# Performance work log

Measured on AMD Instinct MI355X. Metric: run time of the kernel, lower is better.

The kernel has to match this reference:

```python
import jax, jax.numpy as jnp
import numpy as np

NUM_HEADS = 30
EPS = 1e-5


def _fp32_layernorm(x):
    # LayerNorm over last dim, no affine, computed in fp32 (FP32LayerNorm)
    xf = x.astype(jnp.float32)
    mu = jnp.mean(xf, axis=-1, keepdims=True)
    var = jnp.mean(jnp.square(xf - mu), axis=-1, keepdims=True)
    return ((xf - mu) * jax.lax.rsqrt(var + EPS)).astype(x.dtype)


def _apply_rotary(x, cos, sin):
    # x: [B,H,S,hd]; cos/sin: [S,hd] -> broadcast via [None,None]
    half = x.shape[-1] // 2
    xr, xi = x[..., :half], x[..., half:]
    x_rot = jnp.concatenate([-xi, xr], axis=-1)
    out = x.astype(jnp.float32) * cos[None, None] + x_rot.astype(jnp.float32) * sin[None, None]
    return out.astype(x.dtype)


def setup_inputs() -> dict:
    key = jax.random.key(0)
    ks = jax.random.split(key, 12)
    B, S_img, S_txt, D = 1, 3072, 256, 1920
    hd = D // NUM_HEADS
    s = 0.02
    return {
        "hidden_states": jax.random.normal(ks[0], (B, S_img, D), jnp.float32),
        "encoder_hidden_states": jax.random.normal(ks[1], (B, S_txt, D), jnp.float32),
        "rope_cos": jax.random.normal(ks[2], (S_img, hd), jnp.float32),
        "rope_sin": jax.random.normal(ks[3], (S_img, hd), jnp.float32),
        "Wq": jax.random.normal(ks[4], (D, D), jnp.float32) * s,
        "bq": jnp.zeros((D,), jnp.float32),
        "Wk": jax.random.normal(ks[5], (D, D), jnp.float32) * s,
        "bk": jnp.zeros((D,), jnp.float32),
        "Wv": jax.random.normal(ks[6], (D, D), jnp.float32) * s,
        "bv": jnp.zeros((D,), jnp.float32),
        "Wo": jax.random.normal(ks[7], (D, D), jnp.float32) * s,
        "bo": jnp.zeros((D,), jnp.float32),
    }


def reference(hidden_states, encoder_hidden_states, rope_cos, rope_sin,
              Wq, bq, Wk, bk, Wv, bv, Wo, bo):
    T = encoder_hidden_states.shape[1]  # text_seq_length
    x = jnp.concatenate([encoder_hidden_states, hidden_states], axis=1)  # [B,S,D]
    B, S, D = x.shape
    H = NUM_HEADS
    hd = D // H

    def proj(W, b):
        return (x @ W.T + b).reshape(B, S, H, hd).transpose(0, 2, 1, 3)  # [B,H,S,hd]

    q = _fp32_layernorm(proj(Wq, bq))
    k = _fp32_layernorm(proj(Wk, bk))
    v = proj(Wv, bv)

    # partial RoPE: only the image slice (tokens after text)
    q = q.at[:, :, T:, :].set(_apply_rotary(q[:, :, T:, :], rope_cos, rope_sin))
    k = k.at[:, :, T:, :].set(_apply_rotary(k[:, :, T:, :], rope_cos, rope_sin))

    scale = 1.0 / jnp.sqrt(jnp.asarray(hd, q.dtype))
    scores = jnp.einsum("bhqd,bhkd->bhqk", q, k) * scale
    attn = jax.nn.softmax(scores, axis=-1)
    out = jnp.einsum("bhqk,bhkd->bhqd", attn, v)  # [B,H,S,hd]

    out = out.transpose(0, 2, 1, 3).reshape(B, S, D)
    out = out @ Wo.T + bo
    return (out[:, T:], out[:, :T])  # (image hidden_states, encoder_hidden_states)
```

## Files before the change

kernel.cpp:

```cpp
#include <hip/hip_runtime.h>

constexpr int S_TOT  = 3328;
constexpr int S_TXT  = 256;
constexpr int DMODEL = 1920;
constexpr int NHEAD  = 30;
constexpr int HD     = 64;

typedef _Float16 half8 __attribute__((ext_vector_type(8)));
typedef _Float16 half4v __attribute__((ext_vector_type(4)));
typedef float    f32x4 __attribute__((ext_vector_type(4)));
typedef short    bh8   __attribute__((ext_vector_type(8)));

__device__ __forceinline__ f32x4 mfma16h(half8 a, half8 b, f32x4 c) {
    return __builtin_amdgcn_mfma_f32_16x16x32_f16(a, b, c, 0, 0, 0);
}
__device__ __forceinline__ f32x4 mfma16b(bh8 a, bh8 b, f32x4 c) {
    return __builtin_amdgcn_mfma_f32_16x16x32_bf16(a, b, c, 0, 0, 0);
}
__device__ __forceinline__ void gload16(void* lds, const void* g) {
    __builtin_amdgcn_global_load_lds(
        (const __attribute__((address_space(1))) void*)g,
        (__attribute__((address_space(3))) void*)lds, 16, 0, 0);
}

__device__ __forceinline__ unsigned f2u(float x){ union{float f;unsigned u;}c; c.f=x; return c.u; }
__device__ __forceinline__ float u2f(unsigned x){ union{unsigned u;float f;}c; c.u=x; return c.f; }

#define MAXDPP(v, ctrl)                                                        \
    v = fmaxf(v, u2f(__builtin_amdgcn_update_dpp(                              \
            (int)f2u(v), (int)f2u(v), (ctrl), 0xf, 0xf, false)))

__device__ __forceinline__ void split8(const float* p, bh8& hi, bh8& lo) {
    float4 f0 = *(const float4*)p;
    float4 f1 = *(const float4*)(p + 4);
    float f[8] = {f0.x, f0.y, f0.z, f0.w, f1.x, f1.y, f1.z, f1.w};
    union { bh8 v; unsigned short u[8]; } H, L;
    #pragma unroll
    for (int e = 0; e < 8; ++e) {
        unsigned ub = f2u(f[e]);
        H.u[e] = (unsigned short)(ub >> 16);
        float r = f[e] - u2f(ub & 0xFFFF0000u);
        L.u[e] = (unsigned short)(f2u(r) >> 16);
    }
    hi = H.v; lo = L.v;
}

__global__ __launch_bounds__(256) void cvt_xwv(
    const float* __restrict__ hid, const float* __restrict__ enc,
    const float* __restrict__ Wv,
    _Float16* __restrict__ xh, _Float16* __restrict__ Wvh)
{
    const int seg = blockIdx.y;
    const float* src; _Float16* dst; int n;
    switch (seg) {
        case 0:  src = enc; dst = xh;                  n = S_TXT * DMODEL;  break;
        case 1:  src = hid; dst = xh + S_TXT * DMODEL; n = 3072 * DMODEL;   break;
        default: src = Wv;  dst = Wvh;                 n = DMODEL * DMODEL; break;
    }
    for (int i = (blockIdx.x * 256 + threadIdx.x) * 4; i < n; i += gridDim.x * 256 * 4) {
        float4 v = *(const float4*)(src + i);
        half4v h = {(_Float16)v.x, (_Float16)v.y, (_Float16)v.z, (_Float16)v.w};
        *(half4v*)(dst + i) = h;
    }
}

__global__ __launch_bounds__(256) void cvt_wo(const float* __restrict__ Wo,
                                              _Float16* __restrict__ Woh)
{
    const int n = DMODEL * DMODEL;
    for (int i = (blockIdx.x * 256 + threadIdx.x) * 4; i < n; i += gridDim.x * 256 * 4) {
        float4 v = *(const float4*)(Wo + i);
        half4v h = {(_Float16)v.x, (_Float16)v.y, (_Float16)v.z, (_Float16)v.w};
        *(half4v*)(Woh + i) = h;
    }
}

__global__ __launch_bounds__(256) void gemm_v(
    const _Float16* __restrict__ xh,
    const _Float16* __restrict__ Wvh,
    const float* __restrict__ bv,
    _Float16* __restrict__ v_hT)
{
    extern __shared__ __attribute__((aligned(16))) char smem[];
    _Float16* As = (_Float16*)smem;
    _Float16* Bs = (_Float16*)(smem + 8192);

    const int tid  = threadIdx.x;
    const int wave = tid >> 6;
    const int lane = tid & 63;
    const int l16  = lane & 15;
    const int quad = lane >> 4;

    const int m0 = blockIdx.x * 128;
    const int n0 = blockIdx.y * 128;
    const int wm = (wave >> 1) * 64;
    const int wn = (wave & 1) * 64;

    const _Float16* gA = xh  + (size_t)(m0 + wave * 32 + (lane >> 2)) * DMODEL + ((lane & 3) << 3);
    const _Float16* gB = Wvh + (size_t)(n0 + wave * 32 + (lane >> 2)) * DMODEL + ((lane & 3) << 3);
    _Float16* lA = As + wave * 32 * 32;
    _Float16* lB = Bs + wave * 32 * 32;

    f32x4 acc[4][4];
    #pragma unroll
    for (int j = 0; j < 4; ++j)
        #pragma unroll
        for (int i = 0; i < 4; ++i) acc[j][i] = (f32x4){0.f, 0.f, 0.f, 0.f};

    for (int k0 = 0; k0 < DMODEL; k0 += 32) {
        __syncthreads();
        gload16(lA,        gA + k0);
        gload16(lA + 512,  gA + 16 * DMODEL + k0);
        gload16(lB,        gB + k0);
        gload16(lB + 512,  gB + 16 * DMODEL + k0);
        __syncthreads();
        half8 af[4], bf[4];
        #pragma unroll
        for (int j = 0; j < 4; ++j)
            af[j] = *(const half8*)(As + (wm + j * 16 + l16) * 32 + quad * 8);
        #pragma unroll
        for (int i = 0; i < 4; ++i)
            bf[i] = *(const half8*)(Bs + (wn + i * 16 + l16) * 32 + quad * 8);
        #pragma unroll
        for (int j = 0; j < 4; ++j)
            #pragma unroll
            for (int i = 0; i < 4; ++i)
                acc[j][i] = mfma16h(af[j], bf[i], acc[j][i]);
    }
    __syncthreads();

    const int h = (n0 + wn) / 64;
    _Float16* vt = (_Float16*)smem + wave * 64 * 72;
    #pragma unroll
    for (int j = 0; j < 4; ++j)
        #pragma unroll
        for (int r = 0; r < 4; ++r)
            #pragma unroll
            for (int i = 0; i < 4; ++i)
                vt[(i * 16 + l16) * 72 + j * 16 + quad * 4 + r] =
                    (_Float16)(acc[j][i][r] + bv[n0 + wn + i * 16 + l16]);
    __asm__ volatile("" ::: "memory");
    const int dl = lane >> 3;
    const int sl = (lane & 7) << 3;
    #pragma unroll
    for (int t = 0; t < 8; ++t) {
        const int d = t * 8 + dl;
        half8 vv = *(const half8*)(vt + d * 72 + sl);
        *(half8*)(v_hT + (size_t)(h * HD + d) * S_TOT + m0 + wm + sl) = vv;
    }
}

__global__ __launch_bounds__(256) void gemm_qk(
    const float* __restrict__ hid, const float* __restrict__ enc,
    const float* __restrict__ Wq, const float* __restrict__ Wk,
    const float* __restrict__ bq, const float* __restrict__ bk,
    const float* __restrict__ rcos, const float* __restrict__ rsin,
    _Float16* __restrict__ q_h, _Float16* __restrict__ k_h,
    _Float16* __restrict__ q_lo, _Float16* __restrict__ k_lo)
{
    extern __shared__ __attribute__((aligned(16))) char smem[];
    float* As = (float*)smem;
    float* Bs = (float*)(smem + 16384);

    const int tid  = threadIdx.x;
    const int wave = tid >> 6;
    const int lane = tid & 63;
    const int l16  = lane & 15;
    const int quad = lane >> 4;

    const int m0  = blockIdx.x * 128;
    const int n0g = blockIdx.y * 128;
    const int zz  = (n0g >= DMODEL);
    const int nloc = n0g - zz * DMODEL;
    const int wm = (wave >> 1) * 64;
    const int wn = (wave & 1) * 64;

    const float* aSrc = (m0 < S_TXT) ? (enc + (size_t)m0 * DMODEL)
                                     : (hid + (size_t)(m0 - S_TXT) * DMODEL);
    const float* bSrc = (zz ? Wk : Wq) + (size_t)nloc * DMODEL;

    const float* gA = aSrc + (size_t)(wave * 32 + (lane >> 3)) * DMODEL + ((lane & 7) << 2);
    const float* gB = bSrc + (size_t)(wave * 32 + (lane >> 3)) * DMODEL + ((lane & 7) << 2);
    float* lA = As + wave * 32 * 32;
    float* lB = Bs + wave * 32 * 32;

    f32x4 acc[4][4];
    #pragma unroll
    for (int j = 0; j < 4; ++j)
        #pragma unroll
        for (int i = 0; i < 4; ++i) acc[j][i] = (f32x4){0.f, 0.f, 0.f, 0.f};

    for (int k0 = 0; k0 < DMODEL; k0 += 32) {
        __syncthreads();
        #pragma unroll
        for (int t = 0; t < 4; ++t) {
            gload16(lA + t * 256, gA + (size_t)(t * 8) * DMODEL + k0);
            gload16(lB + t * 256, gB + (size_t)(t * 8) * DMODEL + k0);
        }
        __syncthreads();
        bh8 ah[4], al[4], bhv[4], blv[4];
        #pragma unroll
        for (int j = 0; j < 4; ++j)
            split8(As + (wm + j * 16 + l16) * 32 + quad * 8, ah[j], al[j]);
        #pragma unroll
        for (int i = 0; i < 4; ++i)
            split8(Bs + (wn + i * 16 + l16) * 32 + quad * 8, bhv[i], blv[i]);
        #pragma unroll
        for (int j = 0; j < 4; ++j)
            #pragma unroll
            for (int i = 0; i < 4; ++i) {
                acc[j][i] = mfma16b(ah[j], bhv[i], acc[j][i]);
                acc[j][i] = mfma16b(al[j], bhv[i], acc[j][i]);
                acc[j][i] = mfma16b(ah[j], blv[i], acc[j][i]);
            }
    }

    const int h = (nloc + wn) / 64;
    const float* bias = zz ? bk : bq;
    _Float16* dhi = zz ? k_h : q_h;
    _Float16* dlo = zz ? k_lo : q_lo;
    const float qscale = zz ? 1.f : 0.125f;
    const bool rope = (m0 >= S_TXT);

    #pragma unroll
    for (int j = 0; j < 4; ++j) {
        #pragma unroll
        for (int r = 0; r < 4; ++r) {
            const int s = m0 + wm + j * 16 + quad * 4 + r;
            float x[4], s1 = 0.f, s2 = 0.f;
            #pragma unroll
            for (int i = 0; i < 4; ++i) {
                x[i] = acc[j][i][r] + bias[nloc + wn + i * 16 + l16];
                s1 += x[i];
                s2 += x[i] * x[i];
            }
            #pragma unroll
            for (int off = 1; off <= 8; off <<= 1) {
                s1 += __shfl_xor(s1, off);
                s2 += __shfl_xor(s2, off);
            }
            const float mu   = s1 * (1.f / 64.f);
            const float var  = fmaxf(s2 * (1.f / 64.f) - mu * mu, 0.f);
            const float rstd = rsqrtf(var + 1e-5f);
            float xn[4];
            #pragma unroll
            for (int i = 0; i < 4; ++i) xn[i] = (x[i] - mu) * rstd;
            float o[4];
            if (rope) {
                const int pos = s - S_TXT;
                #pragma unroll
                for (int i = 0; i < 4; ++i) {
                    const int d = i * 16 + l16;
                    const float c  = rcos[(size_t)pos * HD + d];
                    const float si = rsin[(size_t)pos * HD + d];
                    const float rot = (i < 2) ? -xn[i ^ 2] : xn[i ^ 2];
                    o[i] = xn[i] * c + rot * si;
                }
            } else {
                #pragma unroll
                for (int i = 0; i < 4; ++i) o[i] = xn[i];
            }
            #pragma unroll
            for (int i = 0; i < 4; ++i) {
                const float vv = o[i] * qscale;
                const _Float16 hv = (_Float16)vv;
                const size_t idx = (size_t)(h * S_TOT + s) * HD + i * 16 + l16;
                dhi[idx] = hv;
                dlo[idx] = (_Float16)((vv - (float)hv) * 1024.f);
            }
        }
    }
}

__global__ __launch_bounds__(256, 3) void attn(
    const _Float16* __restrict__ q_h,  const _Float16* __restrict__ q_lo,
    const _Float16* __restrict__ k_h,  const _Float16* __restrict__ k_lo,
    const _Float16* __restrict__ v_hT,
    _Float16* __restrict__ aout)
{
    extern __shared__ __attribute__((aligned(16))) char smem[];
    _Float16* KsB  = (_Float16*)smem;
    _Float16* KslB = (_Float16*)(smem + 16384);
    _Float16* Vs   = (_Float16*)(smem + 32768);
    _Float16* Pl   = (_Float16*)(smem + 40960);

    const int tid  = threadIdx.x;
    const int wave = tid >> 6;
    const int lane = tid & 63;
    const int l16  = lane & 15;
    const int quad = lane >> 4;
    const int h  = blockIdx.y;
    const int q0 = blockIdx.x * 128 + wave * 32;

    const _Float16* qbase  = q_h  + (size_t)(h * S_TOT + q0) * HD;
    const _Float16* qlbase = q_lo + (size_t)(h * S_TOT + q0) * HD;
    half8 aq0[2], aq1[2], aql0[2], aql1[2];
    #pragma unroll
    for (int j = 0; j < 2; ++j) {
        aq0[j]  = *(const half8*)(qbase  + (j * 16 + l16) * HD + quad * 8);
        aq1[j]  = *(const half8*)(qbase  + (j * 16 + l16) * HD + 32 + quad * 8);
        aql0[j] = *(const half8*)(qlbase + (j * 16 + l16) * HD + quad * 8);
        aql1[j] = *(const half8*)(qlbase + (j * 16 + l16) * HD + 32 + quad * 8);
    }

    const _Float16* kbase  = k_h  + (size_t)h * S_TOT * HD;
    const _Float16* klbase = k_lo + (size_t)h * S_TOT * HD;
    const _Float16* vbase  = v_hT + (size_t)h * HD * S_TOT;

    const int srow = lane >> 3;
    const int schk = ((lane & 7) ^ srow) << 3;
    const _Float16* gK  = kbase  + (size_t)(wave * 16 + srow) * HD + schk;
    const _Float16* gKl = klbase + (size_t)(wave * 16 + srow) * HD + schk;
    const _Float16* gV  = vbase  + (size_t)(wave * 16 + srow) * S_TOT + schk;

    const int c0 = (quad ^ (l16 & 7)) << 3;
    const int c1 = c0 ^ 32;

    f32x4 o[2][4];
    float m_i[2][4], l_i[2][4];
    #pragma unroll
    for (int j = 0; j < 2; ++j)
        #pragma unroll
        for (int i = 0; i < 4; ++i) {
            o[j][i] = (f32x4){0.f, 0.f, 0.f, 0.f};
            m_i[j][i] = -1e30f; l_i[j][i] = 0.f;
        }

    constexpr int NT = S_TOT / 64;

    auto stageK = [&](int kv0, int p) {
        _Float16* lK  = KsB  + p * 4096 + wave * 1024;
        _Float16* lKl = KslB + p * 4096 + wave * 1024;
        gload16(lK,        gK  + (size_t)kv0 * HD);
        gload16(lK + 512,  gK  + (size_t)(kv0 + 8) * HD);
        gload16(lKl,       gKl + (size_t)kv0 * HD);
        gload16(lKl + 512, gKl + (size_t)(kv0 + 8) * HD);
    };
    auto stageV = [&](int kv0) {
        _Float16* lV = Vs + wave * 1024;
        gload16(lV,       gV + kv0);
        gload16(lV + 512, gV + kv0 + 8 * S_TOT);
    };

    stageK(0, 0);
    stageV(0);
    for (int t = 0; t < NT; ++t) {
        const int cur = t & 1;
        if (t + 1 < NT) {
            stageK((t + 1) * 64, cur ^ 1);
            asm volatile("s_waitcnt vmcnt(6)" ::: "memory");
        } else {
            asm volatile("s_waitcnt vmcnt(2)" ::: "memory");
        }
        __builtin_amdgcn_s_barrier();
        const _Float16* Ks  = KsB  + cur * 4096;
        const _Float16* Ksl = KslB + cur * 4096;

        f32x4 sc[2][4];
        #pragma unroll
        for (int i = 0; i < 4; ++i) {
            const int rb = (i * 16 + l16) * 64;
            half8 b0 = *(const half8*)(Ks  + rb + c0);
            half8 b1 = *(const half8*)(Ks  + rb + c1);
            half8 d0 = *(const half8*)(Ksl + rb + c0);
            half8 d1 = *(const half8*)(Ksl + rb + c1);
            #pragma unroll
            for (int j = 0; j < 2; ++j) {
                f32x4 s  = (f32x4){0.f, 0.f, 0.f, 0.f};
                f32x4 s2 = (f32x4){0.f, 0.f, 0.f, 0.f};
                s  = mfma16h(aq0[j],  b0, s);   s  = mfma16h(aq1[j],  b1, s);
                s2 = mfma16h(aql0[j], b0, s2);  s2 = mfma16h(aql1[j], b1, s2);
                s2 = mfma16h(aq0[j],  d0, s2);  s2 = mfma16h(aq1[j],  d1, s2);
                sc[j][i] = s + s2 * 0.0009765625f;
            }
        }
        half8 ap0[2], ap1[2];
        #pragma unroll
        for (int j = 0; j < 2; ++j) {
            #pragma unroll
            for (int r = 0; r < 4; ++r) {
                float mx = fmaxf(fmaxf(sc[j][0][r], sc[j][1][r]),
                                 fmaxf(sc[j][2][r], sc[j][3][r]));
                MAXDPP(mx, 0xB1);
                MAXDPP(mx, 0x4E);
                MAXDPP(mx, 0x124);
                MAXDPP(mx, 0x128);
                const float mnew  = fmaxf(m_i[j][r], mx);
                const float alpha = __expf(m_i[j][r] - mnew);
                m_i[j][r] = mnew;
                float rs = 0.f;
                #pragma unroll
                for (int i = 0; i < 4; ++i) {
                    float p = __expf(sc[j][i][r] - mnew);
                    rs += p;
                    Pl[(wave * 16 + quad * 4 + r) * 72 + i * 16 + l16] = (_Float16)p;
                }
                l_i[j][r] = l_i[j][r] * alpha + rs;
                #pragma unroll
                for (int i = 0; i < 4; ++i) o[j][i][r] *= alpha;
            }
            __asm__ volatile("" ::: "memory");
            ap0[j] = *(const half8*)(Pl + (wave * 16 + l16) * 72 + quad * 8);
            ap1[j] = *(const half8*)(Pl + (wave * 16 + l16) * 72 + 32 + quad * 8);
            __asm__ volatile("" ::: "memory");
        }
        if (t + 1 < NT) asm volatile("s_waitcnt vmcnt(4)" ::: "memory");
        else            asm volatile("s_waitcnt vmcnt(0)" ::: "memory");
        __builtin_amdgcn_s_barrier();
        #pragma unroll
        for (int i = 0; i < 4; ++i) {
            const int rb = (i * 16 + l16) * 64;
            half8 vb0 = *(const half8*)(Vs + rb + c0);
            half8 vb1 = *(const half8*)(Vs + rb + c1);
            #pragma unroll
            for (int j = 0; j < 2; ++j) {
                o[j][i] = mfma16h(ap0[j], vb0, o[j][i]);
                o[j][i] = mfma16h(ap1[j], vb1, o[j][i]);
            }
        }
        asm volatile("s_waitcnt lgkmcnt(0)" ::: "memory");
        __builtin_amdgcn_s_barrier();
        if (t + 1 < NT) stageV((t + 1) * 64);
    }
    #pragma unroll
    for (int j = 0; j < 2; ++j)
        #pragma unroll
        for (int r = 0; r < 4; ++r) {
            float l = l_i[j][r];
            l += __shfl_xor(l, 1);
            l += __shfl_xor(l, 2);
            l += __shfl_xor(l, 4);
            l += __shfl_xor(l, 8);
            const float inv = 1.f / l;
            const int srow2 = q0 + j * 16 + quad * 4 + r;
            #pragma unroll
            for (int i = 0; i < 4; ++i)
                aout[(size_t)srow2 * DMODEL + h * HD + i * 16 + l16] =
                    (_Float16)(o[j][i][r] * inv);
        }
}

__global__ __launch_bounds__(256) void gemm_out(
    const _Float16* __restrict__ A,
    const _Float16* __restrict__ Woh,
    const float* __restrict__ bo,
    float* __restrict__ out)
{
    extern __shared__ __attribute__((aligned(16))) char smem[];
    _Float16* As = (_Float16*)smem;
    _Float16* Bs = (_Float16*)(smem + 8192);

    const int tid  = threadIdx.x;
    const int wave = tid >> 6;
    const int lane = tid & 63;
    const int l16  = lane & 15;
    const int quad = lane >> 4;

    const int m0 = blockIdx.x * 128;
    const int n0 = blockIdx.y * 128;
    const int wm = (wave >> 1) * 64;
    const int wn = (wave & 1) * 64;

    const _Float16* gA = A   + (size_t)(m0 + wave * 32 + (lane >> 2)) * DMODEL + ((lane & 3) << 3);
    const _Float16* gB = Woh + (size_t)(n0 + wave * 32 + (lane >> 2)) * DMODEL + ((lane & 3) << 3);
    _Float16* lA = As + wave * 32 * 32;
    _Float16* lB = Bs + wave * 32 * 32;

    f32x4 acc[4][4];
    #pragma unroll
    for (int j = 0; j < 4; ++j)
        #pragma unroll
        for (int i = 0; i < 4; ++i) acc[j][i] = (f32x4){0.f, 0.f, 0.f, 0.f};

    for (int k0 = 0; k0 < DMODEL; k0 += 32) {
        __syncthreads();
        gload16(lA,        gA + k0);
        gload16(lA + 512,  gA + 16 * DMODEL + k0);
        gload16(lB,        gB + k0);
        gload16(lB + 512,  gB + 16 * DMODEL + k0);
        __syncthreads();
        half8 af[4], bf[4];
        #pragma unroll
        for (int j = 0; j < 4; ++j)
            af[j] = *(const half8*)(As + (wm + j * 16 + l16) * 32 + quad * 8);
        #pragma unroll
        for (int i = 0; i < 4; ++i)
            bf[i] = *(const half8*)(Bs + (wn + i * 16 + l16) * 32 + quad * 8);
        #pragma unroll
        for (int j = 0; j < 4; ++j)
            #pragma unroll
            for (int i = 0; i < 4; ++i)
                acc[j][i] = mfma16h(af[j], bf[i], acc[j][i]);
    }
    #pragma unroll
    for (int j = 0; j < 4; ++j) {
        #pragma unroll
        for (int i = 0; i < 4; ++i) {
            const int n = n0 + wn + i * 16 + l16;
            const float bb = bo[n];
            #pragma unroll
            for (int r = 0; r < 4; ++r) {
                const int m = m0 + wm + j * 16 + quad * 4 + r;
                const int orow = (m >= S_TXT) ? (m - S_TXT) : (m + 3072);
                out[(size_t)orow * DMODEL + n] = acc[j][i][r] + bb;
            }
        }
    }
}

extern "C" void kernel_launch(void* const* d_in, const int* in_sizes, int n_in,
                              void* d_out, int out_size, void* d_ws, size_t ws_size,
                              hipStream_t stream) {
    const float* hid  = (const float*)d_in[0];
    const float* enc  = (const float*)d_in[1];
    const float* rcos = (const float*)d_in[2];
    const float* rsin = (const float*)d_in[3];
    const float* Wq   = (const float*)d_in[4];
    const float* bq   = (const float*)d_in[5];
    const float* Wk   = (const float*)d_in[6];
    const float* bk   = (const float*)d_in[7];
    const float* Wv   = (const float*)d_in[8];
    const float* bv   = (const float*)d_in[9];
    const float* Wo   = (const float*)d_in[10];
    const float* bo   = (const float*)d_in[11];

    char* ws = (char*)d_ws;
    _Float16* xh   = (_Float16*)(ws + 0);
    _Float16* aout = (_Float16*)(ws + 0);
    _Float16* q_h  = (_Float16*)(ws + 12779520);
    _Float16* Woh  = (_Float16*)(ws + 12779520);
    _Float16* k_h  = (_Float16*)(ws + 25559040);
    _Float16* v_hT = (_Float16*)(ws + 38338560);
    _Float16* Wvh  = (_Float16*)d_out;
    _Float16* q_lo = (_Float16*)d_out;
    _Float16* k_lo = (_Float16*)((char*)d_out + 12779520);

    cvt_xwv<<<dim3(128, 3), 256, 0, stream>>>(hid, enc, Wv, xh, Wvh);
    gemm_v<<<dim3(26, 15), 256, 36864, stream>>>(xh, Wvh, bv, v_hT);
    gemm_qk<<<dim3(26, 30), 256, 32768, stream>>>(
        hid, enc, Wq, Wk, bq, bk, rcos, rsin, q_h, k_h, q_lo, k_lo);
    attn<<<dim3(26, NHEAD), 256, 50176, stream>>>(q_h, q_lo, k_h, k_lo, v_hT, aout);
    cvt_wo<<<dim3(128), 256, 0, stream>>>(Wo, Woh);
    gemm_out<<<dim3(26, 15), 256, 16384, stream>>>(aout, Woh, bo, (float*)d_out);
}
```

Measured before the change: 783.6 us.

## Single-buffer K-lo tile, restage after QK, and swizzle P tile to shrink LDS

The attention kernel now keeps only a single LDS buffer for the K low-part tile. That tile is reloaded right after the barrier that follows score computation, so it overlaps the PV MFMAs. The P staging area drops its 72-element padded rows for 64-element rows with an XOR swizzle, and the final-iteration barrier is skipped. Together these cut dynamic LDS from 50176 to 40960 bytes to allow more resident blocks per CU. The trade-off is a shorter prefetch window for K-lo and tighter vmcnt wait accounting.

```diff
diff --git a/kernel.cpp b/kernel.cpp
--- a/kernel.cpp
+++ b/kernel.cpp
@@ -280,9 +280,9 @@
 {
     extern __shared__ __attribute__((aligned(16))) char smem[];
     _Float16* KsB  = (_Float16*)smem;
-    _Float16* KslB = (_Float16*)(smem + 16384);
-    _Float16* Vs   = (_Float16*)(smem + 32768);
-    _Float16* Pl   = (_Float16*)(smem + 40960);
+    _Float16* Ksl  = (_Float16*)(smem + 16384);
+    _Float16* Vs   = (_Float16*)(smem + 24576);
+    _Float16* Pl   = (_Float16*)(smem + 32768);
 
     const int tid  = threadIdx.x;
     const int wave = tid >> 6;
@@ -328,11 +328,13 @@
 
     constexpr int NT = S_TOT / 64;
 
-    auto stageK = [&](int kv0, int p) {
-        _Float16* lK  = KsB  + p * 4096 + wave * 1024;
-        _Float16* lKl = KslB + p * 4096 + wave * 1024;
-        gload16(lK,        gK  + (size_t)kv0 * HD);
-        gload16(lK + 512,  gK  + (size_t)(kv0 + 8) * HD);
+    auto stageKhi = [&](int kv0, int p) {
+        _Float16* lK = KsB + p * 4096 + wave * 1024;
+        gload16(lK,       gK + (size_t)kv0 * HD);
+        gload16(lK + 512, gK + (size_t)(kv0 + 8) * HD);
+    };
+    auto stageKsl = [&](int kv0) {
+        _Float16* lKl = Ksl + wave * 1024;
         gload16(lKl,       gKl + (size_t)kv0 * HD);
         gload16(lKl + 512, gKl + (size_t)(kv0 + 8) * HD);
     };
@@ -342,19 +344,20 @@
         gload16(lV + 512, gV + kv0 + 8 * S_TOT);
     };
 
-    stageK(0, 0);
+    stageKhi(0, 0);
+    stageKsl(0);
     stageV(0);
     for (int t = 0; t < NT; ++t) {
         const int cur = t & 1;
-        if (t + 1 < NT) {
-            stageK((t + 1) * 64, cur ^ 1);
-            asm volatile("s_waitcnt vmcnt(6)" ::: "memory");
+        const bool isLast = (t == NT - 1);
+        if (!isLast) {
+            stageKhi((t + 1) * 64, cur ^ 1);
+            asm volatile("s_waitcnt vmcnt(4)" ::: "memory");
         } else {
             asm volatile("s_waitcnt vmcnt(2)" ::: "memory");
         }
         __builtin_amdgcn_s_barrier();
-        const _Float16* Ks  = KsB  + cur * 4096;
-        const _Float16* Ksl = KslB + cur * 4096;
+        const _Float16* Ks = KsB + cur * 4096;
 
         f32x4 sc[2][4];
         #pragma unroll
@@ -388,25 +391,28 @@
                 const float mnew  = fmaxf(m_i[j][r], mx);
                 const float alpha = __expf(m_i[j][r] - mnew);
                 m_i[j][r] = mnew;
+                const int ro = quad * 4 + r;
+                const int rsw = ((quad & 1) * 4 + r) << 3;
                 float rs = 0.f;
                 #pragma unroll
                 for (int i = 0; i < 4; ++i) {
                     float p = __expf(sc[j][i][r] - mnew);
                     rs += p;
-                    Pl[(wave * 16 + quad * 4 + r) * 72 + i * 16 + l16] = (_Float16)p;
+                    Pl[wave * 1024 + ro * 64 + ((i * 16 + l16) ^ rsw)] = (_Float16)p;
                 }
                 l_i[j][r] = l_i[j][r] * alpha + rs;
                 #pragma unroll
                 for (int i = 0; i < 4; ++i) o[j][i][r] *= alpha;
             }
             __asm__ volatile("" ::: "memory");
-            ap0[j] = *(const half8*)(Pl + (wave * 16 + l16) * 72 + quad * 8);
-            ap1[j] = *(const half8*)(Pl + (wave * 16 + l16) * 72 + 32 + quad * 8);
+            ap0[j] = *(const half8*)(Pl + wave * 1024 + l16 * 64 + c0);
+            ap1[j] = *(const half8*)(Pl + wave * 1024 + l16 * 64 + c1);
             __asm__ volatile("" ::: "memory");
         }
-        if (t + 1 < NT) asm volatile("s_waitcnt vmcnt(4)" ::: "memory");
-        else            asm volatile("s_waitcnt vmcnt(0)" ::: "memory");
+        if (!isLast) asm volatile("s_waitcnt vmcnt(2)" ::: "memory");
+        else         asm volatile("s_waitcnt vmcnt(0)" ::: "memory");
         __builtin_amdgcn_s_barrier();
+        if (!isLast) stageKsl((t + 1) * 64);
         #pragma unroll
         for (int i = 0; i < 4; ++i) {
             const int rb = (i * 16 + l16) * 64;
@@ -418,9 +424,11 @@
                 o[j][i] = mfma16h(ap1[j], vb1, o[j][i]);
             }
         }
-        asm volatile("s_waitcnt lgkmcnt(0)" ::: "memory");
-        __builtin_amdgcn_s_barrier();
-        if (t + 1 < NT) stageV((t + 1) * 64);
+        if (!isLast) {
+            asm volatile("s_waitcnt lgkmcnt(0)" ::: "memory");
+            __builtin_amdgcn_s_barrier();
+            stageV((t + 1) * 64);
+        }
     }
     #pragma unroll
     for (int j = 0; j < 2; ++j)
@@ -539,7 +547,7 @@
     gemm_v<<<dim3(26, 15), 256, 36864, stream>>>(xh, Wvh, bv, v_hT);
     gemm_qk<<<dim3(26, 30), 256, 32768, stream>>>(
         hid, enc, Wq, Wk, bq, bk, rcos, rsin, q_h, k_h, q_lo, k_lo);
-    attn<<<dim3(26, NHEAD), 256, 50176, stream>>>(q_h, q_lo, k_h, k_lo, v_hT, aout);
+    attn<<<dim3(26, NHEAD), 256, 40960, stream>>>(q_h, q_lo, k_h, k_lo, v_hT, aout);
     cvt_wo<<<dim3(128), 256, 0, stream>>>(Wo, Woh);
     gemm_out<<<dim3(26, 15), 256, 16384, stream>>>(aout, Woh, bo, (float*)d_out);
 }
```

After: 792.2 us. Within noise of the previous version (+1.1%).
